# Kernel tuning notes

Measured on AMD Instinct MI355X. Metric: run time of the kernel, lower is better.

## Reference

```python
import jax, jax.numpy as jnp
import numpy as np

KERNEL_MUL = 2.0
KERNEL_NUM = 5


def setup_inputs() -> dict:
    key = jax.random.key(0)
    k1, k2 = jax.random.split(key)
    source = jax.random.normal(k1, (4096, 256), dtype=jnp.float32)
    target = jax.random.normal(k2, (4096, 256), dtype=jnp.float32)
    return {"source": source, "target": target}


def reference(source, target):
    n = source.shape[0]
    total = jnp.concatenate([source, target], axis=0)  # [2N, D]
    n_samples = total.shape[0]
    # Pairwise squared L2 distances via the norms trick (same math as
    # the broadcasted (total0 - total1)**2 sum, without the O(N^2 D) tensor).
    sq = jnp.sum(total * total, axis=-1)  # [2N]
    l2 = sq[:, None] + sq[None, :] - 2.0 * (total @ total.T)  # [2N, 2N]
    # Bandwidth is computed from .data in torch -> detached.
    bandwidth = jax.lax.stop_gradient(jnp.sum(l2)) / (n_samples ** 2 - n_samples)
    bandwidth = bandwidth / (KERNEL_MUL ** (KERNEL_NUM // 2))
    kernels = jnp.zeros_like(l2)
    for i in range(KERNEL_NUM):
        kernels = kernels + jnp.exp(-l2 / (bandwidth * KERNEL_MUL ** i))
    xx = kernels[:n, :n]
    yy = kernels[n:, n:]
    xy = kernels[:n, n:]
    yx = kernels[n:, :n]
    return jnp.mean(xx + yy - xy - yx)
```

## Files before the change

kernel.cpp:

```cpp
#include <hip/hip_runtime.h>
#include <hip/hip_bf16.h>
#if !__has_builtin(__builtin_amdgcn_cvt_pk_fp8_f32)
#include <hip/hip_fp8.h>
#endif

typedef unsigned char u8;
typedef long long i64;
typedef i64 i64x2 __attribute__((ext_vector_type(2)));
typedef float f32x4 __attribute__((ext_vector_type(4)));

#define NROW 8192
#define NHALF 4096
#define DIM 256
#define TILES 64
#define NBLK (TILES * (TILES + 1) / 2)
#define PBLK 512

#define G_COL 0
#define G_SS 256
#define G_CNT1 260
#define G_C4 272
#define G_ACC 288

static __device__ __forceinline__ float fast_exp2(float x) {
#if __has_builtin(__builtin_amdgcn_exp2f)
  return __builtin_amdgcn_exp2f(x);
#else
  return exp2f(x);
#endif
}

static __device__ __forceinline__ unsigned pack4_fp8(float4 v) {
#if __has_builtin(__builtin_amdgcn_cvt_pk_fp8_f32)
  int p = 0;
  p = __builtin_amdgcn_cvt_pk_fp8_f32(v.x, v.y, p, false);
  p = __builtin_amdgcn_cvt_pk_fp8_f32(v.z, v.w, p, true);
  return (unsigned)p;
#else
  __hip_fp8_e4m3 a(v.x), b(v.y), c(v.z), d(v.w);
  return (unsigned)a.__x | ((unsigned)b.__x << 8) | ((unsigned)c.__x << 16) |
         ((unsigned)d.__x << 24);
#endif
}


__global__ void k_prep(const float* __restrict__ src, const float* __restrict__ tgt,
                       u8* __restrict__ Xq, float* __restrict__ sq,
                       float* __restrict__ colpart, float* __restrict__ gbuf) {
  __shared__ float cps[4][DIM];
  int w = threadIdx.x >> 6, lane = threadIdx.x & 63;
  int s = blockIdx.x;
  int cc = threadIdx.x;
  if (s == 0) {
    if (cc <= G_SS) atomicExch(gbuf + cc, 0.f);
    if (cc == 0) atomicExch((unsigned*)(gbuf + G_CNT1), 0u);
    if (cc < 32) atomicExch(gbuf + G_ACC + cc * 16, 0.f);
  }
  int r0 = s * 16 + w * 4;
  int p = lane >> 4, h = (lane >> 3) & 1, q = (lane >> 1) & 3, j = 4 * (lane & 1);
  float4 ca = make_float4(0.f, 0.f, 0.f, 0.f);
#pragma unroll
  for (int rr = 0; rr < 4; ++rr) {
    int row = r0 + rr;
    const float* pp = (row < NHALF) ? (src + (size_t)row * DIM)
                                    : (tgt + (size_t)(row - NHALF) * DIM);
    float4 v = *(const float4*)(pp + lane * 4);
    size_t di = ((size_t)(s * 4 + p) * 64 + q * 16 + (row & 15)) * 16 + h * 8 + j;
    *(unsigned*)(Xq + di) = pack4_fp8(v);
    ca.x += v.x; ca.y += v.y; ca.z += v.z; ca.w += v.w;
    float sum = v.x * v.x + v.y * v.y + v.z * v.z + v.w * v.w;
#pragma unroll
    for (int off = 32; off > 0; off >>= 1) sum += __shfl_down(sum, off);
    if (lane == 0) sq[row] = sum;
  }
  cps[w][lane * 4 + 0] = ca.x;
  cps[w][lane * 4 + 1] = ca.y;
  cps[w][lane * 4 + 2] = ca.z;
  cps[w][lane * 4 + 3] = ca.w;
  __syncthreads();
  colpart[blockIdx.x * DIM + cc] = cps[0][cc] + cps[1][cc] + cps[2][cc] + cps[3][cc];
}

__global__ void k_mid(const float* __restrict__ colpart, const float* __restrict__ sq,
                      float* __restrict__ gbuf) {
  int b = blockIdx.x, c = threadIdx.x, lane = c & 63, w = c >> 6;
  __shared__ float rs[4];
  __shared__ unsigned oldc;
  float s = 0.f;
#pragma unroll
  for (int i = 0; i < 16; ++i) s += colpart[(size_t)(b * 16 + i) * DIM + c];
  atomicAdd(gbuf + G_COL + c, s);
  float qv = sq[b * DIM + c];
#pragma unroll
  for (int off = 32; off > 0; off >>= 1) qv += __shfl_down(qv, off);
  if (lane == 0) rs[w] = qv;
  __syncthreads();
  if (c == 0) {
    atomicAdd(gbuf + G_SS, rs[0] + rs[1] + rs[2] + rs[3]);
    __threadfence();
    oldc = atomicAdd((unsigned*)(gbuf + G_CNT1), 1u);
  }
  __syncthreads();
  if (oldc == 31) {
    float v = atomicAdd(gbuf + G_COL + c, 0.f);
    float vn = v * v;
#pragma unroll
    for (int off = 32; off > 0; off >>= 1) vn += __shfl_down(vn, off);
    __syncthreads();
    if (lane == 0) rs[w] = vn;
    __syncthreads();
    if (c == 0) {
      double VN = (double)rs[0] + rs[1] + rs[2] + rs[3];
      double S  = (double)atomicAdd(gbuf + G_SS, 0.f);
      double suml2 = 2.0 * (double)NROW * S - 2.0 * VN;
      double bw = suml2 / ((double)NROW * NROW - NROW) / 4.0;
      gbuf[G_C4] = (float)(1.4426950408889634 / (bw * 16.0));
    }
  }
}

__global__ __launch_bounds__(256, 4) void k_main(const u8* __restrict__ Xq,
                                                 const float* __restrict__ sq,
                                                 const float* __restrict__ scal,
                                                 float* __restrict__ accbuf) {
  __shared__ float red[4];

  int bi = 0, rem = blockIdx.x;
  while (rem >= TILES - bi) { rem -= TILES - bi; ++bi; }
  int bj = bi + rem;

  int tid = threadIdx.x;
  int w = tid >> 6, lane = tid & 63;
  int wi = w >> 1, wj = w & 1;

  f32x4 acc[4][4];
#pragma unroll
  for (int a = 0; a < 4; ++a)
#pragma unroll
    for (int b = 0; b < 4; ++b) acc[a][b] = (f32x4){0.f, 0.f, 0.f, 0.f};

  const i64x2* X2 = (const i64x2*)Xq;
  const int sA = bi * 8 + wi * 4;
  const int sB = bj * 8 + wj * 4;

#pragma unroll
  for (int p = 0; p < 4; ++p) {
    i64x2 aP[4], bP[4];
#pragma unroll
    for (int mi = 0; mi < 4; ++mi)
      aP[mi] = X2[(size_t)((sA + mi) * 4 + p) * 64 + lane];
#pragma unroll
    for (int ni = 0; ni < 4; ++ni)
      bP[ni] = X2[(size_t)((sB + ni) * 4 + p) * 64 + lane];
#pragma unroll
    for (int mi = 0; mi < 4; ++mi)
#pragma unroll
      for (int ni = 0; ni < 4; ++ni)
        acc[mi][ni] = __builtin_amdgcn_mfma_f32_16x16x32_fp8_fp8(
            aP[mi].x, bP[ni].x, acc[mi][ni], 0, 0, 0);
#pragma unroll
    for (int mi = 0; mi < 4; ++mi)
#pragma unroll
      for (int ni = 0; ni < 4; ++ni)
        acc[mi][ni] = __builtin_amdgcn_mfma_f32_16x16x32_fp8_fp8(
            aP[mi].y, bP[ni].y, acc[mi][ni], 0, 0, 0);
  }

  float c4 = scal[0];
  float wgt = ((bi < 32) == (bj < 32)) ? 1.f : -1.f;
  if (bi != bj) wgt *= 2.f;
  bool diag = (bi == bj);
  int ib = bi * 128 + wi * 64 + (lane >> 4) * 4;
  int jb = bj * 128 + wj * 64 + (lane & 15);
  f32x4 sqi[4];
#pragma unroll
  for (int mi = 0; mi < 4; ++mi) sqi[mi] = *(const f32x4*)(sq + ib + mi * 16);
  float lsum = 0.f;
#pragma unroll
  for (int ni = 0; ni < 4; ++ni) {
    float sqj = sq[jb + ni * 16];
#pragma unroll
    for (int mi = 0; mi < 4; ++mi) {
#pragma unroll
      for (int r = 0; r < 4; ++r) {
        float l2 = sqi[mi][r] + sqj - 2.f * acc[mi][ni][r];
        float t  = fast_exp2(-l2 * c4);
        float t2 = t * t, t4 = t2 * t2, t8 = t4 * t4, t16 = t8 * t8;
        float tt = t + t2 + t4 + t8 + t16;
        if (diag && (ib + mi * 16 + r) == (jb + ni * 16)) tt = 5.f;
        lsum += tt;
      }
    }
  }
#pragma unroll
  for (int off = 32; off > 0; off >>= 1) lsum += __shfl_down(lsum, off);
  if (lane == 0) red[w] = lsum;
  __syncthreads();
  if (tid == 0)
    atomicAdd(accbuf + (blockIdx.x & 31) * 16,
              wgt * (red[0] + red[1] + red[2] + red[3]));
}

__global__ void k_fin(const float* __restrict__ accbuf, float* __restrict__ out) {
  int lane = threadIdx.x & 63;
  float s = (lane < 32) ? accbuf[lane * 16] : 0.f;
#pragma unroll
  for (int off = 32; off > 0; off >>= 1) s += __shfl_down(s, off);
  if (threadIdx.x == 0) out[0] = s / 16777216.f;
}

extern "C" void kernel_launch(void* const* d_in, const int* in_sizes, int n_in,
                              void* d_out, int out_size, void* d_ws, size_t ws_size,
                              hipStream_t stream) {
  const float* src = (const float*)d_in[0];
  const float* tgt = (const float*)d_in[1];
  char* ws = (char*)d_ws;
  u8* Xq = (u8*)ws;
  size_t off = (size_t)NROW * DIM;
  float* sq = (float*)(ws + off);      off += NROW * 4;
  float* colpart = (float*)(ws + off); off += (size_t)PBLK * DIM * 4;
  float* gbuf = (float*)(ws + off);
  float* out = (float*)d_out;

  k_prep<<<PBLK, 256, 0, stream>>>(src, tgt, Xq, sq, colpart, gbuf);
  k_mid<<<32, 256, 0, stream>>>(colpart, sq, gbuf);
  k_main<<<NBLK, 256, 0, stream>>>(Xq, sq, gbuf + G_C4, gbuf + G_ACC);
  k_fin<<<1, 64, 0, stream>>>(gbuf + G_ACC, out);
}
```

Measured before the change: 90.03 us.

## Stage FP8 tiles through LDS and use 16x16x128 scaled MFMA

Reorders the FP8 packed layout so each 1KB chunk holds 16 rows by 16 bytes. The main kernel now stages A and B tiles into shared memory with global_load_lds and feeds the wider mfma_scale 16x16x128 f8f6f4 instruction, replacing many 16x16x32 MFMAs. The epilogue is refolded into one FMA per element by prescaling the squared norms. This adds 32KB of LDS per block, two barriers per K-phase, and lowers the launch-bounds occupancy hint from 4 to 3.

```diff
diff --git a/kernel.cpp b/kernel.cpp
--- a/kernel.cpp
+++ b/kernel.cpp
@@ -5,9 +5,10 @@
 #endif
 
 typedef unsigned char u8;
-typedef long long i64;
-typedef i64 i64x2 __attribute__((ext_vector_type(2)));
 typedef float f32x4 __attribute__((ext_vector_type(4)));
+typedef int v8i __attribute__((ext_vector_type(8)));
+typedef __attribute__((address_space(1))) const void* gas_p;
+typedef __attribute__((address_space(3))) void* las_p;
 
 #define NROW 8192
 #define NHALF 4096
@@ -53,11 +54,12 @@
   int cc = threadIdx.x;
   if (s == 0) {
     if (cc <= G_SS) atomicExch(gbuf + cc, 0.f);
+    if (cc == 0) atomicExch(gbuf + G_SS, 0.f);
     if (cc == 0) atomicExch((unsigned*)(gbuf + G_CNT1), 0u);
     if (cc < 32) atomicExch(gbuf + G_ACC + cc * 16, 0.f);
   }
   int r0 = s * 16 + w * 4;
-  int p = lane >> 4, h = (lane >> 3) & 1, q = (lane >> 1) & 3, j = 4 * (lane & 1);
+  int f = lane >> 5, h2 = (lane >> 2) & 1, g = (lane >> 3) & 3, j4 = (lane & 3) << 2;
   float4 ca = make_float4(0.f, 0.f, 0.f, 0.f);
 #pragma unroll
   for (int rr = 0; rr < 4; ++rr) {
@@ -65,7 +67,8 @@
     const float* pp = (row < NHALF) ? (src + (size_t)row * DIM)
                                     : (tgt + (size_t)(row - NHALF) * DIM);
     float4 v = *(const float4*)(pp + lane * 4);
-    size_t di = ((size_t)(s * 4 + p) * 64 + q * 16 + (row & 15)) * 16 + h * 8 + j;
+    size_t di = ((size_t)(s * 4 + f * 2 + h2) << 10) +
+                ((g * 16 + (row & 15)) << 4) + j4;
     *(unsigned*)(Xq + di) = pack4_fp8(v);
     ca.x += v.x; ca.y += v.y; ca.z += v.z; ca.w += v.w;
     float sum = v.x * v.x + v.y * v.y + v.z * v.z + v.w * v.w;
@@ -119,10 +122,11 @@
   }
 }
 
-__global__ __launch_bounds__(256, 4) void k_main(const u8* __restrict__ Xq,
+__global__ __launch_bounds__(256, 3) void k_main(const u8* __restrict__ Xq,
                                                  const float* __restrict__ sq,
                                                  const float* __restrict__ scal,
                                                  float* __restrict__ accbuf) {
+  __shared__ u8 stage[32768];
   __shared__ float red[4];
 
   int bi = 0, rem = blockIdx.x;
@@ -139,52 +143,67 @@
 #pragma unroll
     for (int b = 0; b < 4; ++b) acc[a][b] = (f32x4){0.f, 0.f, 0.f, 0.f};
 
-  const i64x2* X2 = (const i64x2*)Xq;
-  const int sA = bi * 8 + wi * 4;
-  const int sB = bj * 8 + wj * 4;
-
-#pragma unroll
-  for (int p = 0; p < 4; ++p) {
-    i64x2 aP[4], bP[4];
+#pragma unroll
+  for (int f = 0; f < 2; ++f) {
+#pragma unroll
+    for (int i = 0; i < 8; ++i) {
+      int c = w + i * 4;
+      int ii = c & 15;
+      int bb = (c < 16) ? bi : bj;
+      int gchunk = (bb * 8 + (ii >> 1)) * 4 + f * 2 + (ii & 1);
+      const u8* g = Xq + ((size_t)gchunk << 10) + lane * 16;
+      __builtin_amdgcn_global_load_lds((gas_p)g, (las_p)(stage + (c << 10)),
+                                       16, 0, 0);
+    }
+    __syncthreads();
+
+    v8i aV[4], bV[4];
+#pragma unroll
+    for (int mi = 0; mi < 4; ++mi) {
+      const u8* base = stage + ((wi * 4 + mi) << 11) + lane * 16;
+      int4 lo = *(const int4*)(base);
+      int4 hi = *(const int4*)(base + 1024);
+      aV[mi] = (v8i){lo.x, lo.y, lo.z, lo.w, hi.x, hi.y, hi.z, hi.w};
+    }
+#pragma unroll
+    for (int ni = 0; ni < 4; ++ni) {
+      const u8* base = stage + 16384 + ((wj * 4 + ni) << 11) + lane * 16;
+      int4 lo = *(const int4*)(base);
+      int4 hi = *(const int4*)(base + 1024);
+      bV[ni] = (v8i){lo.x, lo.y, lo.z, lo.w, hi.x, hi.y, hi.z, hi.w};
+    }
 #pragma unroll
     for (int mi = 0; mi < 4; ++mi)
-      aP[mi] = X2[(size_t)((sA + mi) * 4 + p) * 64 + lane];
-#pragma unroll
-    for (int ni = 0; ni < 4; ++ni)
-      bP[ni] = X2[(size_t)((sB + ni) * 4 + p) * 64 + lane];
-#pragma unroll
-    for (int mi = 0; mi < 4; ++mi)
 #pragma unroll
       for (int ni = 0; ni < 4; ++ni)
-        acc[mi][ni] = __builtin_amdgcn_mfma_f32_16x16x32_fp8_fp8(
-            aP[mi].x, bP[ni].x, acc[mi][ni], 0, 0, 0);
-#pragma unroll
-    for (int mi = 0; mi < 4; ++mi)
-#pragma unroll
-      for (int ni = 0; ni < 4; ++ni)
-        acc[mi][ni] = __builtin_amdgcn_mfma_f32_16x16x32_fp8_fp8(
-            aP[mi].y, bP[ni].y, acc[mi][ni], 0, 0, 0);
+        acc[mi][ni] = __builtin_amdgcn_mfma_scale_f32_16x16x128_f8f6f4(
+            aV[mi], bV[ni], acc[mi][ni], 0 , 0 ,
+            0, 0x7f7f7f7f, 0, 0x7f7f7f7f);
+    __syncthreads();
   }
 
   float c4 = scal[0];
+  float c2 = 2.f * c4;
   float wgt = ((bi < 32) == (bj < 32)) ? 1.f : -1.f;
   if (bi != bj) wgt *= 2.f;
   bool diag = (bi == bj);
   int ib = bi * 128 + wi * 64 + (lane >> 4) * 4;
   int jb = bj * 128 + wj * 64 + (lane & 15);
-  f32x4 sqi[4];
-#pragma unroll
-  for (int mi = 0; mi < 4; ++mi) sqi[mi] = *(const f32x4*)(sq + ib + mi * 16);
+  f32x4 sic[4];
+#pragma unroll
+  for (int mi = 0; mi < 4; ++mi) {
+    f32x4 q = *(const f32x4*)(sq + ib + mi * 16);
+    sic[mi] = q * (-c4);
+  }
   float lsum = 0.f;
 #pragma unroll
   for (int ni = 0; ni < 4; ++ni) {
-    float sqj = sq[jb + ni * 16];
+    float sjc = sq[jb + ni * 16] * (-c4);
 #pragma unroll
     for (int mi = 0; mi < 4; ++mi) {
 #pragma unroll
       for (int r = 0; r < 4; ++r) {
-        float l2 = sqi[mi][r] + sqj - 2.f * acc[mi][ni][r];
-        float t  = fast_exp2(-l2 * c4);
+        float t  = fast_exp2(__builtin_fmaf(acc[mi][ni][r], c2, sic[mi][r] + sjc));
         float t2 = t * t, t4 = t2 * t2, t8 = t4 * t4, t16 = t8 * t8;
         float tt = t + t2 + t4 + t8 + t16;
         if (diag && (ib + mi * 16 + r) == (jb + ni * 16)) tt = 5.f;
```

Measured after the change: 90.56 us. No clear change (+0.6%).
